# Kernel optimization log

Measured on AMD Instinct MI355X. Metric: run time of the kernel, lower is better.

The kernel has to match this reference:

```python
import jax, jax.numpy as jnp
import numpy as np

N = 50000   # nodes
E = 800000  # edges
F = 16      # raw feature width (sliced 4:10 -> 6)
H = 256     # hidden_dim
O = 128     # out_dim
NE = 4      # n_experts
G = 64      # graphs in batch
K = 2       # top_k
XS, XE = 4, 10
SPS = 0.3   # size_prior_strength


def setup_inputs() -> dict:
    key = jax.random.key(0)
    ks = jax.random.split(key, 16)
    rn = lambda k, s: jax.random.normal(k, s, dtype=jnp.float32) * 0.05
    return dict(
        x=jax.random.normal(ks[0], (N, F), dtype=jnp.float32),
        edge_index=jax.random.randint(ks[1], (2, E), 0, N),
        batch=jnp.sort(jax.random.randint(ks[2], (N,), 0, G)),
        enc_W1=rn(ks[3], (6, H)), enc_b1=jnp.zeros(H, jnp.float32),
        enc_W2=rn(ks[4], (H, H)), enc_b2=jnp.zeros(H, jnp.float32),
        r_W1=rn(ks[5], (H + 3, H)), r_b1=jnp.zeros(H, jnp.float32),
        ln_g=jnp.ones(H, jnp.float32), ln_b=jnp.zeros(H, jnp.float32),
        r_W2=rn(ks[6], (H, NE)), r_b2=jnp.zeros(NE, jnp.float32),
        size_centers=jnp.linspace(0.0, 1.0, NE, dtype=jnp.float32),
        W0_rel=rn(ks[7], (NE, H, H)), b0_rel=jnp.zeros((NE, H), jnp.float32), W0_root=rn(ks[8], (NE, H, H)),
        W1_rel=rn(ks[9], (NE, H, H)), b1_rel=jnp.zeros((NE, H), jnp.float32), W1_root=rn(ks[10], (NE, H, H)),
        W2_rel=rn(ks[11], (NE, H, O)), b2_rel=jnp.zeros((NE, O), jnp.float32), W2_root=rn(ks[12], (NE, H, O)),
    )


def _forward(x, edge_index, batch, enc_W1, enc_b1, enc_W2, enc_b2,
             r_W1, r_b1, ln_g, ln_b, r_W2, r_b2, size_centers,
             W0_rel, b0_rel, W0_root, W1_rel, b1_rel, W1_root, W2_rel, b2_rel, W2_root):
    src, dst = edge_index[0], edge_index[1]
    xs = x[:, XS:XE]                                   # [N,6]
    h = jax.nn.relu(xs @ enc_W1 + enc_b1) @ enc_W2 + enc_b2  # [N,H]

    # per-graph size features (bincounts via scatter-add)
    n = jnp.maximum(jnp.zeros(G, jnp.float32).at[batch].add(1.0), 1.0)
    e = jnp.zeros(G, jnp.float32).at[batch[src]].add(1.0)
    density = e / jnp.maximum(n * (n - 1.0), 1.0)
    logn = jnp.log(n)
    logn_norm = (logn - logn.min()) / (logn.max() - logn.min() + 1e-6)
    feats = jnp.stack([n, e, density], -1)             # [G,3]
    feats = (feats - feats.mean(0, keepdims=True)) / (feats.std(0, keepdims=True) + 1e-6)
    sf = feats[batch]                                   # [N,3]
    ln_node = logn_norm[batch]                          # [N]

    # router: Linear -> LayerNorm -> ReLU -> Linear, combined with size prior
    inp = jnp.concatenate([h, sf], -1)                  # [N,H+3]
    t = inp @ r_W1 + r_b1
    t = (t - t.mean(-1, keepdims=True)) * jax.lax.rsqrt(t.var(-1, keepdims=True) + 1e-5) * ln_g + ln_b
    learned = jax.nn.relu(t) @ r_W2 + r_b2              # [N,NE]
    prior = -(ln_node[:, None] - size_centers[None, :]) ** 2
    logits = (1.0 - SPS) * learned + SPS * prior        # temperature = 1.0

    # top-k gate
    probs = jax.nn.softmax(logits, -1)
    top_vals, top_idx = jax.lax.top_k(probs, K)
    top_vals = top_vals / (top_vals.sum(-1, keepdims=True) + 1e-8)
    weights = jnp.zeros_like(probs).at[jnp.arange(N)[:, None], top_idx].set(top_vals)

    # GraphConv experts: out = lin_rel(sum_{j->i} x_j) + lin_root(x_i)
    def aggregate(v):  # [N,C] -> [N,C] scatter-add of src features onto dst
        return jnp.zeros_like(v).at[dst].add(v[src])

    agg_h = aggregate(h)
    hE = jax.nn.relu(jnp.einsum('nh,eho->eno', agg_h, W0_rel) + b0_rel[:, None, :]
                     + jnp.einsum('nh,eho->eno', h, W0_root))            # [NE,N,H]
    aggE = jax.vmap(aggregate)(hE)
    hE = jax.nn.relu(jnp.einsum('enh,eho->eno', aggE, W1_rel) + b1_rel[:, None, :]
                     + jnp.einsum('enh,eho->eno', hE, W1_root))          # [NE,N,H]
    aggE = jax.vmap(aggregate)(hE)
    outE = (jnp.einsum('enh,eho->eno', aggE, W2_rel) + b2_rel[:, None, :]
            + jnp.einsum('enh,eho->eno', hE, W2_root))                   # [NE,N,O]

    return jnp.einsum('eno,ne->no', outE, weights)                       # [N,O]


def reference(x, edge_index, batch, enc_W1, enc_b1, enc_W2, enc_b2,
              r_W1, r_b1, ln_g, ln_b, r_W2, r_b2, size_centers,
              W0_rel, b0_rel, W0_root, W1_rel, b1_rel, W1_root, W2_rel, b2_rel, W2_root):
    return _forward(x, edge_index, batch, enc_W1, enc_b1, enc_W2, enc_b2,
                    r_W1, r_b1, ln_g, ln_b, r_W2, r_b2, size_centers,
                    W0_rel, b0_rel, W0_root, W1_rel, b1_rel, W1_root, W2_rel, b2_rel, W2_root)
```

## Files before the change

### kernel.cpp

```cpp
#include <hip/hip_runtime.h>
#include <hip/hip_bf16.h>

#define H_DIM 256
#define O_DIM 128
#define NEXP 4
#define G_DIM 64

typedef unsigned short ushort_t;
typedef unsigned int uint_t;
typedef __attribute__((ext_vector_type(8))) short short8;
typedef __attribute__((ext_vector_type(4))) float floatx4;

__device__ __forceinline__ float bf2f(ushort_t u) {
    union { uint_t i; float f; } c; c.i = ((uint_t)u) << 16; return c.f;
}
__device__ __forceinline__ ushort_t f2bf(float f) {
    union { float f; uint_t i; } c; c.f = f;
    uint_t x = c.i;
    uint_t r = (x + 0x7fffu + ((x >> 16) & 1u)) >> 16;
    return (ushort_t)r;
}

__device__ __forceinline__ void load16_lds(const void* g, void* l) {
    __builtin_amdgcn_global_load_lds(
        (const __attribute__((address_space(1))) unsigned int*)g,
        (__attribute__((address_space(3))) unsigned int*)l, 16, 0, 0);
}

__global__ void zero_i_kernel(int* __restrict__ p, long n) {
    long i = (long)blockIdx.x * blockDim.x + threadIdx.x;
    if (i < n) p[i] = 0;
}

__global__ void wsplit2_kernel(const float* __restrict__ Wa, const float* __restrict__ Wb,
                               ushort_t* __restrict__ Wh) {
    int z = blockIdx.y;
    int i = blockIdx.x * 256 + threadIdx.x;
    if (i >= 131072) return;
    int nn = i >> 9, kk = i & 511;
    float v = (kk < 256) ? Wa[(long)z * 65536 + kk * 256 + nn]
                         : Wb[(long)z * 65536 + (kk - 256) * 256 + nn];
    Wh[(long)z * 131072 + i] = f2bf(v);
}

__global__ void wsplitcat_kernel(const float* __restrict__ Wa, const float* __restrict__ Wb,
                                 ushort_t* __restrict__ Wh) {
    int z = blockIdx.y;
    int i = blockIdx.x * 256 + threadIdx.x;
    if (i >= 65536) return;
    int nn = i >> 8, kk = i & 255;
    float v = (nn < 128) ? Wa[(long)z * 32768 + kk * 128 + nn]
                         : Wb[(long)z * 32768 + kk * 128 + (nn - 128)];
    Wh[(long)z * 65536 + i] = f2bf(v);
}

__global__ void encoder1_kernel(const float* __restrict__ x, const float* __restrict__ W1,
                                const float* __restrict__ b1, float* __restrict__ u,
                                int N, int F) {
    int n = blockIdx.x;
    int j = threadIdx.x;
    float acc = b1[j];
    #pragma unroll
    for (int c = 0; c < 6; ++c)
        acc += x[(long)n * F + 4 + c] * W1[c * H_DIM + j];
    u[(long)n * H_DIM + j] = fmaxf(acc, 0.f);
}

__global__ __launch_bounds__(256)
void gemm256_kernel(const float* __restrict__ A, const float* __restrict__ W,
                    const float* __restrict__ bias, float* __restrict__ C,
                    ushort_t* __restrict__ Cbf, int M, int Nc) {
    const int K = 256;
    __shared__ float As[16][68];
    __shared__ float Ws[16][68];
    int tid = threadIdx.x;
    int tx = tid & 15, ty = tid >> 4;
    int row0 = blockIdx.x * 64;
    int col0 = blockIdx.y * 64;
    float acc[4][4] = {};
    int lrow = tid >> 2, kq = tid & 3;
    int wk = tid >> 4, wc = (tid & 15) * 4;
    for (int k0 = 0; k0 < K; k0 += 16) {
        float4 av = make_float4(0.f, 0.f, 0.f, 0.f);
        int arow = row0 + lrow;
        if (arow < M) av = *(const float4*)(A + (long)arow * K + k0 + kq * 4);
        As[kq * 4 + 0][lrow] = av.x;
        As[kq * 4 + 1][lrow] = av.y;
        As[kq * 4 + 2][lrow] = av.z;
        As[kq * 4 + 3][lrow] = av.w;
        float4 wv = *(const float4*)(W + (long)(k0 + wk) * Nc + col0 + wc);
        *(float4*)&Ws[wk][wc] = wv;
        __syncthreads();
        #pragma unroll
        for (int kk = 0; kk < 16; ++kk) {
            float a[4], b[4];
            #pragma unroll
            for (int i = 0; i < 4; ++i) a[i] = As[kk][ty * 4 + i];
            #pragma unroll
            for (int j = 0; j < 4; ++j) b[j] = Ws[kk][tx * 4 + j];
            #pragma unroll
            for (int i = 0; i < 4; ++i)
                #pragma unroll
                for (int j = 0; j < 4; ++j) acc[i][j] += a[i] * b[j];
        }
        __syncthreads();
    }
    #pragma unroll
    for (int i = 0; i < 4; ++i) {
        int r = row0 + ty * 4 + i;
        if (r >= M) break;
        #pragma unroll
        for (int j = 0; j < 4; ++j) {
            int c = col0 + tx * 4 + j;
            float v = acc[i][j];
            if (bias) v += bias[c];
            C[(long)r * Nc + c] = v;
            if (Cbf) Cbf[(long)r * Nc + c] = f2bf(v);
        }
    }
}

template<int NH>
__global__ __launch_bounds__(256)
void gemm_bf_kernel(const ushort_t* __restrict__ A1, long sA1z, int rsA1,
                    const ushort_t* __restrict__ A2, long sA2z, int rsA2,
                    const ushort_t* __restrict__ B, long sBz,
                    const float* __restrict__ bias, int sBiasz,
                    ushort_t* __restrict__ Cbf, long sCz, int rsC,
                    int M, int Kb, int relu) {
    __shared__ alignas(16) ushort_t Asl[128 * 32];
    __shared__ alignas(16) ushort_t Bsl[128 * 32];

    const int tid = threadIdx.x, wave = tid >> 6, lane = tid & 63;
    const int z = blockIdx.z;
    const int row0 = blockIdx.x * 128, col0 = blockIdx.y * 128;
    const int wr = (wave >> 1) * 64, wcx = (wave & 1) * 64;
    floatx4 acc[4][4] = {};

    A1 += (long)z * sA1z;
    A2 += (long)z * sA2z;
    B += (long)z * sBz;
    if (bias) bias += (long)z * sBiasz;
    Cbf += (long)z * sCz;

    const int bsr = lane >> 2;
    const int bgc = ((lane & 3) - (bsr >> 1)) & 3;
    long aoff1[2], aoff2[2];
    #pragma unroll
    for (int q = 0; q < 2; ++q) {
        int ar = row0 + wave * 32 + q * 16 + bsr;
        ar = ar < M ? ar : M - 1;
        aoff1[q] = (long)ar * rsA1 + bgc * 8;
        aoff2[q] = (long)ar * rsA2 + bgc * 8;
    }
    const long brow = (long)(col0 + wave * 32 + bsr) * Kb + bgc * 8;
    const ushort_t* Bg0 = B + brow;
    const ushort_t* Bg1 = B + brow + (long)16 * Kb;
    ushort_t* Al0 = &Asl[(wave * 32) * 32];
    ushort_t* Al1 = &Asl[(wave * 32 + 16) * 32];
    ushort_t* Bl0 = &Bsl[(wave * 32) * 32];
    ushort_t* Bl1 = &Bsl[(wave * 32 + 16) * 32];

    const int fm = lane & 15, fq = lane >> 4;

    #pragma unroll
    for (int half = 0; half < NH; ++half) {
        const ushort_t* Ab = (half == 0) ? A1 : A2;
        const long* aoff = (half == 0) ? aoff1 : aoff2;
        for (int k0 = 0; k0 < 256; k0 += 32) {
            const int kk = half * 256 + k0;
            load16_lds(Ab + aoff[0] + k0, Al0);
            load16_lds(Ab + aoff[1] + k0, Al1);
            load16_lds(Bg0 + kk, Bl0);
            load16_lds(Bg1 + kk, Bl1);
            __syncthreads();

            short8 a[4], b[4];
            #pragma unroll
            for (int j = 0; j < 4; ++j) {
                int row = wcx + j * 16 + fm;
                int slot = (fq + ((row >> 1) & 3)) & 3;
                b[j] = *(const short8*)&Bsl[row * 32 + slot * 8];
            }
            #pragma unroll
            for (int i = 0; i < 4; ++i) {
                int row = wr + i * 16 + fm;
                int slot = (fq + ((row >> 1) & 3)) & 3;
                a[i] = *(const short8*)&Asl[row * 32 + slot * 8];
            }
            #pragma unroll
            for (int i = 0; i < 4; ++i)
                #pragma unroll
                for (int j = 0; j < 4; ++j)
                    acc[i][j] = __builtin_amdgcn_mfma_f32_16x16x32_bf16(a[i], b[j], acc[i][j], 0, 0, 0);
            __syncthreads();
        }
    }

    #pragma unroll
    for (int i = 0; i < 4; ++i) {
        #pragma unroll
        for (int j = 0; j < 4; ++j) {
            int col = col0 + wcx + j * 16 + fm;
            int rowb = row0 + wr + i * 16 + fq * 4;
            #pragma unroll
            for (int r = 0; r < 4; ++r) {
                int row = rowb + r;
                if (row < M) {
                    float v = acc[i][j][r];
                    if (bias) v += bias[col];
                    if (relu) v = fmaxf(v, 0.f);
                    Cbf[(long)row * rsC + col] = f2bf(v);
                }
            }
        }
    }
}

__global__ void hist_nodes_kernel(const int* __restrict__ batch, int n, int* __restrict__ gn) {
    __shared__ int bins[G_DIM];
    int t = threadIdx.x;
    if (t < G_DIM) bins[t] = 0;
    __syncthreads();
    for (long i = (long)blockIdx.x * blockDim.x + t; i < n; i += (long)gridDim.x * blockDim.x)
        atomicAdd(&bins[batch[i]], 1);
    __syncthreads();
    if (t < G_DIM) atomicAdd(&gn[t], bins[t]);
}

__global__ void hist_edges_kernel(const int* __restrict__ ei, const int* __restrict__ batch,
                                  int E, int* __restrict__ ge) {
    __shared__ int bins[G_DIM];
    int t = threadIdx.x;
    if (t < G_DIM) bins[t] = 0;
    __syncthreads();
    for (long i = (long)blockIdx.x * blockDim.x + t; i < E; i += (long)gridDim.x * blockDim.x)
        atomicAdd(&bins[batch[ei[i]]], 1);
    __syncthreads();
    if (t < G_DIM) atomicAdd(&ge[t], bins[t]);
}

__global__ void graph_stats_kernel(const int* __restrict__ gn, const int* __restrict__ ge,
                                   float* __restrict__ feats_norm, float* __restrict__ logn_norm) {
    int g = threadIdx.x;
    float nv = fmaxf((float)gn[g], 1.0f);
    float ev = (float)ge[g];
    float density = ev / fmaxf(nv * (nv - 1.0f), 1.0f);
    float logn = logf(nv);
    float mn = logn, mx = logn;
    for (int o = 32; o; o >>= 1) {
        mn = fminf(mn, __shfl_xor(mn, o));
        mx = fmaxf(mx, __shfl_xor(mx, o));
    }
    logn_norm[g] = (logn - mn) / (mx - mn + 1e-6f);
    float f[3] = {nv, ev, density};
    #pragma unroll
    for (int c = 0; c < 3; ++c) {
        float s = f[c];
        for (int o = 32; o; o >>= 1) s += __shfl_xor(s, o);
        float mean = s / 64.f;
        float d = f[c] - mean;
        float v = d * d;
        for (int o = 32; o; o >>= 1) v += __shfl_xor(v, o);
        float stdv = sqrtf(v / 64.f);
        feats_norm[g * 3 + c] = d / (stdv + 1e-6f);
    }
}

__global__ __launch_bounds__(256)
void router_epi_kernel(const float* __restrict__ t, const int* __restrict__ batch,
                       const float* __restrict__ feats_norm, const float* __restrict__ logn_norm,
                       const float* __restrict__ rW1, const float* __restrict__ rb1,
                       const float* __restrict__ lng, const float* __restrict__ lnb,
                       const float* __restrict__ rW2, const float* __restrict__ rb2,
                       const float* __restrict__ centers, float* __restrict__ w, int N) {
    int wave = threadIdx.x >> 6, lane = threadIdx.x & 63;
    int n = blockIdx.x * 4 + wave;
    if (n >= N) return;
    int g = batch[n];
    float sf0 = feats_norm[g * 3 + 0], sf1 = feats_norm[g * 3 + 1], sf2 = feats_norm[g * 3 + 2];
    float ln = logn_norm[g];
    float tv[4];
    #pragma unroll
    for (int q = 0; q < 4; ++q) {
        int j = lane + 64 * q;
        tv[q] = t[(long)n * H_DIM + j] + rb1[j]
              + sf0 * rW1[256 * H_DIM + j] + sf1 * rW1[257 * H_DIM + j] + sf2 * rW1[258 * H_DIM + j];
    }
    float s = tv[0] + tv[1] + tv[2] + tv[3];
    for (int o = 32; o; o >>= 1) s += __shfl_xor(s, o);
    float mean = s / 256.f;
    float vs = 0.f;
    #pragma unroll
    for (int q = 0; q < 4; ++q) { float d = tv[q] - mean; vs += d * d; }
    for (int o = 32; o; o >>= 1) vs += __shfl_xor(vs, o);
    float rstd = rsqrtf(vs / 256.f + 1e-5f);
    float le[NEXP] = {0.f, 0.f, 0.f, 0.f};
    #pragma unroll
    for (int q = 0; q < 4; ++q) {
        int j = lane + 64 * q;
        float y = (tv[q] - mean) * rstd * lng[j] + lnb[j];
        y = fmaxf(y, 0.f);
        #pragma unroll
        for (int e = 0; e < NEXP; ++e) le[e] += y * rW2[j * NEXP + e];
    }
    #pragma unroll
    for (int e = 0; e < NEXP; ++e)
        for (int o = 32; o; o >>= 1) le[e] += __shfl_xor(le[e], o);
    if (lane == 0) {
        float p[NEXP];
        float m = -1e30f;
        #pragma unroll
        for (int e = 0; e < NEXP; ++e) {
            float d = ln - centers[e];
            float lv = 0.7f * (le[e] + rb2[e]) + 0.3f * (-(d * d));
            p[e] = lv;
            m = fmaxf(m, lv);
        }
        float ssum = 0.f;
        #pragma unroll
        for (int e = 0; e < NEXP; ++e) { p[e] = expf(p[e] - m); ssum += p[e]; }
        #pragma unroll
        for (int e = 0; e < NEXP; ++e) p[e] /= ssum;
        int i1 = 0;
        for (int e = 1; e < NEXP; ++e) if (p[e] > p[i1]) i1 = e;
        int i2 = -1;
        for (int e = 0; e < NEXP; ++e) { if (e == i1) continue; if (i2 < 0 || p[e] > p[i2]) i2 = e; }
        float denom = p[i1] + p[i2] + 1e-8f;
        float out4[NEXP] = {0.f, 0.f, 0.f, 0.f};
        out4[i1] = p[i1] / denom;
        out4[i2] = p[i2] / denom;
        #pragma unroll
        for (int e = 0; e < NEXP; ++e) w[(long)n * NEXP + e] = out4[e];
    }
}

__global__ void count_dst_kernel(const int* __restrict__ ei, int E, int* __restrict__ cnt) {
    int i = blockIdx.x * blockDim.x + threadIdx.x;
    if (i < E) atomicAdd(&cnt[ei[E + i]], 1);
}

__global__ __launch_bounds__(1024)
void scan_kernel(const int* __restrict__ cnt, int* __restrict__ row_ptr, int n) {
    __shared__ int buf[1024];
    __shared__ int carry_s;
    int tid = threadIdx.x;
    if (tid == 0) carry_s = 0;
    __syncthreads();
    for (int base = 0; base < n; base += 1024) {
        int v = (base + tid < n) ? cnt[base + tid] : 0;
        buf[tid] = v;
        __syncthreads();
        for (int off = 1; off < 1024; off <<= 1) {
            int tv = (tid >= off) ? buf[tid - off] : 0;
            __syncthreads();
            buf[tid] += tv;
            __syncthreads();
        }
        int carry = carry_s;
        if (base + tid < n) row_ptr[base + tid] = carry + buf[tid] - v;
        __syncthreads();
        if (tid == 1023) carry_s = carry + buf[1023];
        __syncthreads();
    }
    if (tid == 0) row_ptr[n] = carry_s;
}

__global__ void fill_csr_kernel(const int* __restrict__ ei, int E, const int* __restrict__ row_ptr,
                                int* __restrict__ fillc, int* __restrict__ srcs) {
    int i = blockIdx.x * blockDim.x + threadIdx.x;
    if (i < E) {
        int d = ei[E + i];
        int pos = row_ptr[d] + atomicAdd(&fillc[d], 1);
        srcs[pos] = ei[i];
    }
}

__global__ __launch_bounds__(256)
void agg_b2b_kernel(const ushort_t* __restrict__ feat, ushort_t* __restrict__ outp,
                    const int* __restrict__ rp, const int* __restrict__ srcs, int N) {
    int wave = threadIdx.x >> 6, lane = threadIdx.x & 63;
    int n = blockIdx.x * 4 + wave;
    if (n >= N) return;
    float a0 = 0.f, a1 = 0.f, a2 = 0.f, a3 = 0.f;
    int p0 = rp[n], p1 = rp[n + 1];
    const ushort_t* base = feat + lane * 4;
    int p = p0;
    for (; p + 3 < p1; p += 4) {
        uint2 v0 = *(const uint2*)(base + (long)srcs[p] * H_DIM);
        uint2 v1 = *(const uint2*)(base + (long)srcs[p + 1] * H_DIM);
        uint2 v2 = *(const uint2*)(base + (long)srcs[p + 2] * H_DIM);
        uint2 v3 = *(const uint2*)(base + (long)srcs[p + 3] * H_DIM);
        a0 += bf2f((ushort_t)(v0.x & 0xffff)) + bf2f((ushort_t)(v1.x & 0xffff))
            + bf2f((ushort_t)(v2.x & 0xffff)) + bf2f((ushort_t)(v3.x & 0xffff));
        a1 += bf2f((ushort_t)(v0.x >> 16)) + bf2f((ushort_t)(v1.x >> 16))
            + bf2f((ushort_t)(v2.x >> 16)) + bf2f((ushort_t)(v3.x >> 16));
        a2 += bf2f((ushort_t)(v0.y & 0xffff)) + bf2f((ushort_t)(v1.y & 0xffff))
            + bf2f((ushort_t)(v2.y & 0xffff)) + bf2f((ushort_t)(v3.y & 0xffff));
        a3 += bf2f((ushort_t)(v0.y >> 16)) + bf2f((ushort_t)(v1.y >> 16))
            + bf2f((ushort_t)(v2.y >> 16)) + bf2f((ushort_t)(v3.y >> 16));
    }
    for (; p < p1; ++p) {
        uint2 v = *(const uint2*)(base + (long)srcs[p] * H_DIM);
        a0 += bf2f((ushort_t)(v.x & 0xffff));
        a1 += bf2f((ushort_t)(v.x >> 16));
        a2 += bf2f((ushort_t)(v.y & 0xffff));
        a3 += bf2f((ushort_t)(v.y >> 16));
    }
    uint2 o;
    o.x = (uint_t)f2bf(a0) | ((uint_t)f2bf(a1) << 16);
    o.y = (uint_t)f2bf(a2) | ((uint_t)f2bf(a3) << 16);
    *(uint2*)(outp + (long)n * H_DIM + lane * 4) = o;
}

__global__ void aggI_kernel(const ushort_t* __restrict__ feat, ushort_t* __restrict__ outp,
                            const int* __restrict__ rp, const int* __restrict__ srcs,
                            int N, int W) {
    int n = blockIdx.x;
    int t = threadIdx.x;
    float a0 = 0.f, a1 = 0.f, a2 = 0.f, a3 = 0.f;
    int p0 = rp[n], p1 = rp[n + 1];
    const ushort_t* base = feat + t * 4;
    int p = p0;
    for (; p + 3 < p1; p += 4) {
        uint2 v0 = *(const uint2*)(base + (long)srcs[p] * W);
        uint2 v1 = *(const uint2*)(base + (long)srcs[p + 1] * W);
        uint2 v2 = *(const uint2*)(base + (long)srcs[p + 2] * W);
        uint2 v3 = *(const uint2*)(base + (long)srcs[p + 3] * W);
        a0 += bf2f((ushort_t)(v0.x & 0xffff)) + bf2f((ushort_t)(v1.x & 0xffff))
            + bf2f((ushort_t)(v2.x & 0xffff)) + bf2f((ushort_t)(v3.x & 0xffff));
        a1 += bf2f((ushort_t)(v0.x >> 16)) + bf2f((ushort_t)(v1.x >> 16))
            + bf2f((ushort_t)(v2.x >> 16)) + bf2f((ushort_t)(v3.x >> 16));
        a2 += bf2f((ushort_t)(v0.y & 0xffff)) + bf2f((ushort_t)(v1.y & 0xffff))
            + bf2f((ushort_t)(v2.y & 0xffff)) + bf2f((ushort_t)(v3.y & 0xffff));
        a3 += bf2f((ushort_t)(v0.y >> 16)) + bf2f((ushort_t)(v1.y >> 16))
            + bf2f((ushort_t)(v2.y >> 16)) + bf2f((ushort_t)(v3.y >> 16));
    }
    for (; p < p1; ++p) {
        uint2 v = *(const uint2*)(base + (long)srcs[p] * W);
        a0 += bf2f((ushort_t)(v.x & 0xffff));
        a1 += bf2f((ushort_t)(v.x >> 16));
        a2 += bf2f((ushort_t)(v.y & 0xffff));
        a3 += bf2f((ushort_t)(v.y >> 16));
    }
    uint2 o;
    o.x = (uint_t)f2bf(a0) | ((uint_t)f2bf(a1) << 16);
    o.y = (uint_t)f2bf(a2) | ((uint_t)f2bf(a3) << 16);
    *(uint2*)(outp + (long)n * W + t * 4) = o;
}

__global__ __launch_bounds__(256)
void final_mixE_kernel(const ushort_t* __restrict__ PR, const float* __restrict__ b2,
                       const float* __restrict__ wts, int e0, int EB,
                       const int* __restrict__ rp, const int* __restrict__ srcs,
                       float* __restrict__ out, int N, int init) {
    int wave = threadIdx.x >> 6, lane = threadIdx.x & 63;
    int n = blockIdx.x * 4 + wave;
    if (n >= N) return;
    const int W = EB * 256;
    int c0 = lane * 2;
    long obase = (long)n * O_DIM + c0;
    float o0 = init ? 0.f : out[obase];
    float o1 = init ? 0.f : out[obase + 1];
    int zs[2]; float wv[2]; int na = 0;
    for (int z = 0; z < EB; ++z) {
        float w = wts[(long)n * NEXP + e0 + z];
        if (w != 0.f && na < 2) { zs[na] = z; wv[na] = w; ++na; }
    }
    if (na) {
        const ushort_t* P0 = PR + zs[0] * 256 + c0;
        const ushort_t* P1 = PR + zs[na - 1] * 256 + c0;
        float a00 = 0.f, a01 = 0.f, a10 = 0.f, a11 = 0.f;
        int p0 = rp[n], p1 = rp[n + 1];
        if (na == 2) {
            int p = p0;
            for (; p + 1 < p1; p += 2) {
                long s0 = (long)srcs[p] * W;
                long s1 = (long)srcs[p + 1] * W;
                uint_t v00 = *(const uint_t*)(P0 + s0);
                uint_t v10 = *(const uint_t*)(P1 + s0);
                uint_t v01 = *(const uint_t*)(P0 + s1);
                uint_t v11 = *(const uint_t*)(P1 + s1);
                a00 += bf2f((ushort_t)(v00 & 0xffff)) + bf2f((ushort_t)(v01 & 0xffff));
                a01 += bf2f((ushort_t)(v00 >> 16))    + bf2f((ushort_t)(v01 >> 16));
                a10 += bf2f((ushort_t)(v10 & 0xffff)) + bf2f((ushort_t)(v11 & 0xffff));
                a11 += bf2f((ushort_t)(v10 >> 16))    + bf2f((ushort_t)(v11 >> 16));
            }
            if (p < p1) {
                long s = (long)srcs[p] * W;
                uint_t v0 = *(const uint_t*)(P0 + s);
                uint_t v1 = *(const uint_t*)(P1 + s);
                a00 += bf2f((ushort_t)(v0 & 0xffff)); a01 += bf2f((ushort_t)(v0 >> 16));
                a10 += bf2f((ushort_t)(v1 & 0xffff)); a11 += bf2f((ushort_t)(v1 >> 16));
            }
        } else {
            int p = p0;
            for (; p + 3 < p1; p += 4) {
                uint_t v0 = *(const uint_t*)(P0 + (long)srcs[p] * W);
                uint_t v1 = *(const uint_t*)(P0 + (long)srcs[p + 1] * W);
                uint_t v2 = *(const uint_t*)(P0 + (long)srcs[p + 2] * W);
                uint_t v3 = *(const uint_t*)(P0 + (long)srcs[p + 3] * W);
                a00 += bf2f((ushort_t)(v0 & 0xffff)) + bf2f((ushort_t)(v1 & 0xffff))
                     + bf2f((ushort_t)(v2 & 0xffff)) + bf2f((ushort_t)(v3 & 0xffff));
                a01 += bf2f((ushort_t)(v0 >> 16)) + bf2f((ushort_t)(v1 >> 16))
                     + bf2f((ushort_t)(v2 >> 16)) + bf2f((ushort_t)(v3 >> 16));
            }
            for (; p < p1; ++p) {
                uint_t v = *(const uint_t*)(P0 + (long)srcs[p] * W);
                a00 += bf2f((ushort_t)(v & 0xffff)); a01 += bf2f((ushort_t)(v >> 16));
            }
        }
        {
            int e = e0 + zs[0];
            uint_t rv = *(const uint_t*)(PR + (long)n * W + zs[0] * 256 + 128 + c0);
            o0 += wv[0] * (a00 + bf2f((ushort_t)(rv & 0xffff)) + b2[e * O_DIM + c0]);
            o1 += wv[0] * (a01 + bf2f((ushort_t)(rv >> 16))    + b2[e * O_DIM + c0 + 1]);
        }
        if (na == 2) {
            int e = e0 + zs[1];
            uint_t rv = *(const uint_t*)(PR + (long)n * W + zs[1] * 256 + 128 + c0);
            o0 += wv[1] * (a10 + bf2f((ushort_t)(rv & 0xffff)) + b2[e * O_DIM + c0]);
            o1 += wv[1] * (a11 + bf2f((ushort_t)(rv >> 16))    + b2[e * O_DIM + c0 + 1]);
        }
    }
    out[obase] = o0;
    out[obase + 1] = o1;
}

extern "C" void kernel_launch(void* const* d_in, const int* in_sizes, int n_in,
                              void* d_out, int out_size, void* d_ws, size_t ws_size,
                              hipStream_t stream) {
    const float* x       = (const float*)d_in[0];
    const int*   ei      = (const int*)  d_in[1];
    const int*   batch   = (const int*)  d_in[2];
    const float* enc_W1  = (const float*)d_in[3];
    const float* enc_b1  = (const float*)d_in[4];
    const float* enc_W2  = (const float*)d_in[5];
    const float* enc_b2  = (const float*)d_in[6];
    const float* r_W1    = (const float*)d_in[7];
    const float* r_b1    = (const float*)d_in[8];
    const float* ln_g    = (const float*)d_in[9];
    const float* ln_b    = (const float*)d_in[10];
    const float* r_W2    = (const float*)d_in[11];
    const float* r_b2    = (const float*)d_in[12];
    const float* centers = (const float*)d_in[13];
    const float* W0_rel  = (const float*)d_in[14];
    const float* b0_rel  = (const float*)d_in[15];
    const float* W0_root = (const float*)d_in[16];
    const float* W1_rel  = (const float*)d_in[17];
    const float* b1_rel  = (const float*)d_in[18];
    const float* W1_root = (const float*)d_in[19];
    const float* W2_rel  = (const float*)d_in[20];
    const float* b2_rel  = (const float*)d_in[21];
    const float* W2_root = (const float*)d_in[22];

    const int N = in_sizes[2];
    const int E = in_sizes[1] / 2;
    const int F = in_sizes[0] / N;

    char* ws = (char*)d_ws;
    size_t off = 0;
    auto alloc = [&](size_t bytes) -> void* {
        void* p = ws + off;
        off += (bytes + 255) & ~(size_t)255;
        return p;
    };
    int* cnt      = (int*)alloc((size_t)N * 4);
    int* fillc    = (int*)alloc((size_t)N * 4);
    int* gn       = (int*)alloc((size_t)G_DIM * 4);
    int* ge       = (int*)alloc((size_t)G_DIM * 4);
    size_t zero_bytes = off;
    int* row_ptr  = (int*)alloc((size_t)(N + 1) * 4);
    int* srcs     = (int*)alloc((size_t)E * 4);
    float* feats_norm = (float*)alloc((size_t)G_DIM * 3 * 4);
    float* logn_norm  = (float*)alloc((size_t)G_DIM * 4);
    float* wts    = (float*)alloc((size_t)N * NEXP * 4);
    ushort_t* wf0  = (ushort_t*)alloc((size_t)NEXP * 131072 * 2);
    ushort_t* wf1  = (ushort_t*)alloc((size_t)NEXP * 131072 * 2);
    ushort_t* wfin = (ushort_t*)alloc((size_t)NEXP * 65536 * 2);
    const long sE = (long)N * H_DIM;
    ushort_t* h_bf    = (ushort_t*)alloc((size_t)sE * 2);
    ushort_t* aggh_bf = (ushort_t*)alloc((size_t)sE * 2);
    size_t fixed_end = off;
    size_t slab4 = ((size_t)4 * sE * 2 + 255) & ~(size_t)255;
    int EB = (ws_size >= fixed_end + 3 * slab4 + (1u << 20)) ? 4 : 2;
    size_t slab = ((size_t)EB * sE * 2 + 255) & ~(size_t)255;
    ushort_t* S1 = (ushort_t*)alloc(slab);
    ushort_t* S2 = (ushort_t*)alloc(slab);
    ushort_t* S3 = (ushort_t*)alloc(slab);
    (void)out_size; (void)n_in;

    float* u    = (float*)S1;
    float* h    = (float*)S2;
    float* tf32 = (float*)S3;
    ushort_t* hE0  = S1;
    ushort_t* aggE = S2;
    ushort_t* hE1  = S3;
    ushort_t* PR   = S2;
    float* out = (float*)d_out;

    const int W  = EB * 256;
    dim3 blk256(256);
    dim3 gR((N + 63) / 64, H_DIM / 64, 1);
    dim3 gM((N + 127) / 128, 2, EB);
    dim3 gAgg((N + 3) / 4);

    {
        long nz = (long)(zero_bytes / 4);
        zero_i_kernel<<<dim3((nz + 255) / 256), blk256, 0, stream>>>((int*)ws, nz);
    }
    wsplit2_kernel<<<dim3(512, NEXP), blk256, 0, stream>>>(W0_rel, W0_root, wf0);
    wsplit2_kernel<<<dim3(512, NEXP), blk256, 0, stream>>>(W1_rel, W1_root, wf1);
    wsplitcat_kernel<<<dim3(256, NEXP), blk256, 0, stream>>>(W2_rel, W2_root, wfin);
    encoder1_kernel<<<dim3(N), blk256, 0, stream>>>(x, enc_W1, enc_b1, u, N, F);
    gemm256_kernel<<<gR, blk256, 0, stream>>>(u, enc_W2, enc_b2, h, h_bf, N, H_DIM);
    hist_nodes_kernel<<<dim3(256), blk256, 0, stream>>>(batch, N, gn);
    hist_edges_kernel<<<dim3(512), blk256, 0, stream>>>(ei, batch, E, ge);
    graph_stats_kernel<<<dim3(1), dim3(64), 0, stream>>>(gn, ge, feats_norm, logn_norm);
    gemm256_kernel<<<gR, blk256, 0, stream>>>(h, r_W1, nullptr, tf32, nullptr, N, H_DIM);
    router_epi_kernel<<<dim3((N + 3) / 4), blk256, 0, stream>>>(
        tf32, batch, feats_norm, logn_norm, r_W1, r_b1, ln_g, ln_b, r_W2, r_b2, centers, wts, N);
    count_dst_kernel<<<dim3((E + 255) / 256), blk256, 0, stream>>>(ei, E, cnt);
    scan_kernel<<<dim3(1), dim3(1024), 0, stream>>>(cnt, row_ptr, N);
    fill_csr_kernel<<<dim3((E + 255) / 256), blk256, 0, stream>>>(ei, E, row_ptr, fillc, srcs);
    agg_b2b_kernel<<<gAgg, blk256, 0, stream>>>(h_bf, aggh_bf, row_ptr, srcs, N);

    for (int b = 0; b < NEXP / EB; ++b) {
        const int e0 = b * EB;
        gemm_bf_kernel<2><<<gM, blk256, 0, stream>>>(
            aggh_bf, 0, 256, h_bf, 0, 256,
            wf0 + (long)e0 * 131072, 131072,
            b0_rel + e0 * H_DIM, H_DIM, hE0, 256, W, N, 512, 1);
        aggI_kernel<<<dim3(N), dim3(W / 4), 0, stream>>>(hE0, aggE, row_ptr, srcs, N, W);
        gemm_bf_kernel<2><<<gM, blk256, 0, stream>>>(
            aggE, 256, W, hE0, 256, W,
            wf1 + (long)e0 * 131072, 131072,
            b1_rel + e0 * H_DIM, H_DIM, hE1, 256, W, N, 512, 1);
        gemm_bf_kernel<1><<<gM, blk256, 0, stream>>>(
            hE1, 256, W, nullptr, 0, 256,
            wfin + (long)e0 * 65536, 65536,
            nullptr, 0, PR, 256, W, N, 256, 0);
        final_mixE_kernel<<<gAgg, blk256, 0, stream>>>(
            PR, b2_rel, wts, e0, EB, row_ptr, srcs, out, N, b == 0 ? 1 : 0);
    }
}
```

Baseline: 1.306 ms.

## Double-buffer LDS in bf16 GEMM and widen aggregation loads to 16 bytes

The bf16 MFMA GEMM now uses two LDS buffers, prefetching the next K tile while computing the current one, so each K step needs one barrier instead of two. The goal is to overlap global-to-LDS loads with MFMA work. The expert aggregation kernel now has each thread load 8 bf16 values with uint4 instead of 4 with uint2, halving the thread count and widening memory transactions. The LDS footprint doubles, which may reduce occupancy.

```diff
diff --git a/kernel.cpp b/kernel.cpp
--- a/kernel.cpp
+++ b/kernel.cpp
@@ -128,8 +128,8 @@
                     const float* __restrict__ bias, int sBiasz,
                     ushort_t* __restrict__ Cbf, long sCz, int rsC,
                     int M, int Kb, int relu) {
-    __shared__ alignas(16) ushort_t Asl[128 * 32];
-    __shared__ alignas(16) ushort_t Bsl[128 * 32];
+    __shared__ alignas(16) ushort_t Asl[2][128 * 32];
+    __shared__ alignas(16) ushort_t Bsl[2][128 * 32];
 
     const int tid = threadIdx.x, wave = tid >> 6, lane = tid & 63;
     const int z = blockIdx.z;
@@ -156,45 +156,50 @@
     const long brow = (long)(col0 + wave * 32 + bsr) * Kb + bgc * 8;
     const ushort_t* Bg0 = B + brow;
     const ushort_t* Bg1 = B + brow + (long)16 * Kb;
-    ushort_t* Al0 = &Asl[(wave * 32) * 32];
-    ushort_t* Al1 = &Asl[(wave * 32 + 16) * 32];
-    ushort_t* Bl0 = &Bsl[(wave * 32) * 32];
-    ushort_t* Bl1 = &Bsl[(wave * 32 + 16) * 32];
+    const int la0 = (wave * 32) * 32;
+    const int la1 = (wave * 32 + 16) * 32;
 
     const int fm = lane & 15, fq = lane >> 4;
-
-    #pragma unroll
-    for (int half = 0; half < NH; ++half) {
-        const ushort_t* Ab = (half == 0) ? A1 : A2;
-        const long* aoff = (half == 0) ? aoff1 : aoff2;
-        for (int k0 = 0; k0 < 256; k0 += 32) {
-            const int kk = half * 256 + k0;
-            load16_lds(Ab + aoff[0] + k0, Al0);
-            load16_lds(Ab + aoff[1] + k0, Al1);
-            load16_lds(Bg0 + kk, Bl0);
-            load16_lds(Bg1 + kk, Bl1);
-            __syncthreads();
-
-            short8 a[4], b[4];
+    const int NK = NH * 8;
+
+    load16_lds(A1 + aoff1[0], &Asl[0][la0]);
+    load16_lds(A1 + aoff1[1], &Asl[0][la1]);
+    load16_lds(Bg0, &Bsl[0][la0]);
+    load16_lds(Bg1, &Bsl[0][la1]);
+    __syncthreads();
+
+    for (int k = 0; k < NK; ++k) {
+        const int buf = k & 1;
+        short8 a[4], b[4];
+        #pragma unroll
+        for (int j = 0; j < 4; ++j) {
+            int row = wcx + j * 16 + fm;
+            int slot = (fq + ((row >> 1) & 3)) & 3;
+            b[j] = *(const short8*)&Bsl[buf][row * 32 + slot * 8];
+        }
+        #pragma unroll
+        for (int i = 0; i < 4; ++i) {
+            int row = wr + i * 16 + fm;
+            int slot = (fq + ((row >> 1) & 3)) & 3;
+            a[i] = *(const short8*)&Asl[buf][row * 32 + slot * 8];
+        }
+        if (k + 1 < NK) {
+            const int kn = k + 1, bn = kn & 1;
+            const ushort_t* Ab = (kn >> 3) ? A2 : A1;
+            const long* ao = (kn >> 3) ? aoff2 : aoff1;
+            const int k0 = (kn & 7) * 32;
+            const int kk = kn * 32;
+            load16_lds(Ab + ao[0] + k0, &Asl[bn][la0]);
+            load16_lds(Ab + ao[1] + k0, &Asl[bn][la1]);
+            load16_lds(Bg0 + kk, &Bsl[bn][la0]);
+            load16_lds(Bg1 + kk, &Bsl[bn][la1]);
+        }
+        #pragma unroll
+        for (int i = 0; i < 4; ++i)
             #pragma unroll
-            for (int j = 0; j < 4; ++j) {
-                int row = wcx + j * 16 + fm;
-                int slot = (fq + ((row >> 1) & 3)) & 3;
-                b[j] = *(const short8*)&Bsl[row * 32 + slot * 8];
-            }
-            #pragma unroll
-            for (int i = 0; i < 4; ++i) {
-                int row = wr + i * 16 + fm;
-                int slot = (fq + ((row >> 1) & 3)) & 3;
-                a[i] = *(const short8*)&Asl[row * 32 + slot * 8];
-            }
-            #pragma unroll
-            for (int i = 0; i < 4; ++i)
-                #pragma unroll
-                for (int j = 0; j < 4; ++j)
-                    acc[i][j] = __builtin_amdgcn_mfma_f32_16x16x32_bf16(a[i], b[j], acc[i][j], 0, 0, 0);
-            __syncthreads();
-        }
+            for (int j = 0; j < 4; ++j)
+                acc[i][j] = __builtin_amdgcn_mfma_f32_16x16x32_bf16(a[i], b[j], acc[i][j], 0, 0, 0);
+        if (k + 1 < NK) __syncthreads();
     }
 
     #pragma unroll
@@ -418,35 +423,42 @@
                             int N, int W) {
     int n = blockIdx.x;
     int t = threadIdx.x;
-    float a0 = 0.f, a1 = 0.f, a2 = 0.f, a3 = 0.f;
+    float a[8] = {0.f, 0.f, 0.f, 0.f, 0.f, 0.f, 0.f, 0.f};
     int p0 = rp[n], p1 = rp[n + 1];
-    const ushort_t* base = feat + t * 4;
+    const ushort_t* base = feat + t * 8;
     int p = p0;
     for (; p + 3 < p1; p += 4) {
-        uint2 v0 = *(const uint2*)(base + (long)srcs[p] * W);
-        uint2 v1 = *(const uint2*)(base + (long)srcs[p + 1] * W);
-        uint2 v2 = *(const uint2*)(base + (long)srcs[p + 2] * W);
-        uint2 v3 = *(const uint2*)(base + (long)srcs[p + 3] * W);
-        a0 += bf2f((ushort_t)(v0.x & 0xffff)) + bf2f((ushort_t)(v1.x & 0xffff))
-            + bf2f((ushort_t)(v2.x & 0xffff)) + bf2f((ushort_t)(v3.x & 0xffff));
-        a1 += bf2f((ushort_t)(v0.x >> 16)) + bf2f((ushort_t)(v1.x >> 16))
-            + bf2f((ushort_t)(v2.x >> 16)) + bf2f((ushort_t)(v3.x >> 16));
-        a2 += bf2f((ushort_t)(v0.y & 0xffff)) + bf2f((ushort_t)(v1.y & 0xffff))
-            + bf2f((ushort_t)(v2.y & 0xffff)) + bf2f((ushort_t)(v3.y & 0xffff));
-        a3 += bf2f((ushort_t)(v0.y >> 16)) + bf2f((ushort_t)(v1.y >> 16))
-            + bf2f((ushort_t)(v2.y >> 16)) + bf2f((ushort_t)(v3.y >> 16));
+        uint4 v0 = *(const uint4*)(base + (long)srcs[p] * W);
+        uint4 v1 = *(const uint4*)(base + (long)srcs[p + 1] * W);
+        uint4 v2 = *(const uint4*)(base + (long)srcs[p + 2] * W);
+        uint4 v3 = *(const uint4*)(base + (long)srcs[p + 3] * W);
+        uint_t w0[4] = {v0.x, v0.y, v0.z, v0.w};
+        uint_t w1[4] = {v1.x, v1.y, v1.z, v1.w};
+        uint_t w2[4] = {v2.x, v2.y, v2.z, v2.w};
+        uint_t w3[4] = {v3.x, v3.y, v3.z, v3.w};
+        #pragma unroll
+        for (int q = 0; q < 4; ++q) {
+            a[2 * q]     += bf2f((ushort_t)(w0[q] & 0xffff)) + bf2f((ushort_t)(w1[q] & 0xffff))
+                          + bf2f((ushort_t)(w2[q] & 0xffff)) + bf2f((ushort_t)(w3[q] & 0xffff));
+            a[2 * q + 1] += bf2f((ushort_t)(w0[q] >> 16)) + bf2f((ushort_t)(w1[q] >> 16))
+                          + bf2f((ushort_t)(w2[q] >> 16)) + bf2f((ushort_t)(w3[q] >> 16));
+        }
     }
     for (; p < p1; ++p) {
-        uint2 v = *(const uint2*)(base + (long)srcs[p] * W);
-        a0 += bf2f((ushort_t)(v.x & 0xffff));
-        a1 += bf2f((ushort_t)(v.x >> 16));
-        a2 += bf2f((ushort_t)(v.y & 0xffff));
-        a3 += bf2f((ushort_t)(v.y >> 16));
-    }
-    uint2 o;
-    o.x = (uint_t)f2bf(a0) | ((uint_t)f2bf(a1) << 16);
-    o.y = (uint_t)f2bf(a2) | ((uint_t)f2bf(a3) << 16);
-    *(uint2*)(outp + (long)n * W + t * 4) = o;
+        uint4 v = *(const uint4*)(base + (long)srcs[p] * W);
+        uint_t w[4] = {v.x, v.y, v.z, v.w};
+        #pragma unroll
+        for (int q = 0; q < 4; ++q) {
+            a[2 * q]     += bf2f((ushort_t)(w[q] & 0xffff));
+            a[2 * q + 1] += bf2f((ushort_t)(w[q] >> 16));
+        }
+    }
+    uint4 o;
+    o.x = (uint_t)f2bf(a[0]) | ((uint_t)f2bf(a[1]) << 16);
+    o.y = (uint_t)f2bf(a[2]) | ((uint_t)f2bf(a[3]) << 16);
+    o.z = (uint_t)f2bf(a[4]) | ((uint_t)f2bf(a[5]) << 16);
+    o.w = (uint_t)f2bf(a[6]) | ((uint_t)f2bf(a[7]) << 16);
+    *(uint4*)(outp + (long)n * W + t * 8) = o;
 }
 
 __global__ __launch_bounds__(256)
@@ -631,7 +643,7 @@
             aggh_bf, 0, 256, h_bf, 0, 256,
             wf0 + (long)e0 * 131072, 131072,
             b0_rel + e0 * H_DIM, H_DIM, hE0, 256, W, N, 512, 1);
-        aggI_kernel<<<dim3(N), dim3(W / 4), 0, stream>>>(hE0, aggE, row_ptr, srcs, N, W);
+        aggI_kernel<<<dim3(N), dim3(W / 8), 0, stream>>>(hE0, aggE, row_ptr, srcs, N, W);
         gemm_bf_kernel<2><<<gM, blk256, 0, stream>>>(
             aggE, 256, W, hE0, 256, W,
             wf1 + (long)e0 * 131072, 131072,
```

After: 1.294 ms. No clear change (-0.9%).
